# Kernel optimization log

Hardware: AMD Instinct MI355X
Metric: run time of the kernel (lower is better)

Reference implementation:

```python
import jax, jax.numpy as jnp
import numpy as np

B, T, C = 16, 4096, 256


def setup_inputs() -> dict:
    key = jax.random.key(0)
    kx, kl = jax.random.split(key)
    x = jax.random.normal(kx, (B, T, C), dtype=jnp.float32)
    lengths = jax.random.randint(kl, (B,), T // 2, T + 1)  # valid lengths per sample
    pool_ranges = lengths  # region to pool over; k <= pool_range guaranteed by layer/total_layers choice
    return {
        "x": x,
        "lengths": lengths,
        "pool_ranges": pool_ranges,
        "top_k": 4,
        "layer": 1,
        "total_layers": 4,
    }


def _pool_one(xb, k, pool_range):
    # xb: [T, C]; keep, per column independently, the k largest values among the
    # first pool_range rows, preserving original row order (torch kmax_pooling).
    Trows, Ccols = xb.shape
    valid = jnp.arange(Trows) < pool_range            # [T]
    vals = jnp.where(valid[:, None], xb, -jnp.inf)    # mask invalid rows to rank last
    order = jnp.argsort(-vals, axis=0)                # descending order per column
    rank = jnp.argsort(order, axis=0)                 # inverse permutation = rank of each row
    keep = (rank < k) & valid[:, None]                # [T, C] which entries survive
    pos = jnp.cumsum(keep.astype(jnp.int32), axis=0) - 1  # compacted output row per column
    idx = jnp.where(keep, pos, Trows)                 # dropped entries -> dummy row Trows
    cols = jnp.arange(Ccols)[None, :]
    out = jnp.zeros((Trows + 1, Ccols), xb.dtype).at[idx, cols].set(
        jnp.where(keep, xb, jnp.zeros((), xb.dtype))
    )
    return out[:-1]                                   # [T, C]; rows >= k are zero padding


def reference(x, lengths, pool_ranges, top_k, layer, total_layers):
    # pool_target = max(top_k, ceil((total_layers - layer)/total_layers * length))
    num = total_layers - layer
    k = jnp.maximum(top_k, (num * lengths + total_layers - 1) // total_layers)
    k = jnp.minimum(k, pool_ranges)  # topk requires k <= available rows
    results = jax.vmap(_pool_one)(x, k, pool_ranges)  # [B, T, C], zero-padded past k_i
    pool_result_ranges = k
    return results, pool_result_ranges
```

## Files before the change

kernel.cpp:

```cpp
#include <hip/hip_runtime.h>
#include <stdint.h>


constexpr int T_ROWS = 4096;
constexpr int C_COLS = 256;
constexpr int NBATCH = 16;
constexpr int NSUB   = 8;
constexpr size_t NTOT = (size_t)NBATCH * T_ROWS * C_COLS;

__device__ __forceinline__ int compute_k(const int* lengths, const int* pool_ranges,
                                         const int* p_top_k, const int* p_layer,
                                         const int* p_total, int b, int* pr_out)
{
    int pr = pool_ranges[b];
    pr = pr < 0 ? 0 : (pr > T_ROWS ? T_ROWS : pr);
    const int len   = lengths[b];
    const int top_k = p_top_k[0];
    const int tot   = p_total[0];
    const int num   = tot - p_layer[0];
    int k = (num * len + tot - 1) / tot;
    if (k < top_k) k = top_k;
    if (k > pr)    k = pr;
    *pr_out = pr;
    return k;
}

__global__ __launch_bounds__(256)
void transpose_key_kernel(const float* __restrict__ x, uint32_t* __restrict__ xT)
{
    __shared__ uint32_t tile[64][65];
    const int bid = blockIdx.x;
    const int b   = bid >> 8;
    const int tt  = (bid >> 2) & 63;
    const int ct  = bid & 3;
    const int t0  = tt * 64, c0 = ct * 64;
    const int tid = threadIdx.x;
    const int qq  = tid & 15;
    const int rr  = tid >> 4;

    #pragma unroll
    for (int it = 0; it < 4; ++it) {
        const int r = it * 16 + rr;
        const float4 v = *reinterpret_cast<const float4*>(
            x + ((size_t)(b * T_ROWS + t0 + r) << 8) + c0 + qq * 4);
        const uint32_t w4[4] = {__float_as_uint(v.x), __float_as_uint(v.y),
                                __float_as_uint(v.z), __float_as_uint(v.w)};
        #pragma unroll
        for (int j = 0; j < 4; ++j)
            tile[qq * 4 + j][r] = w4[j] ^ ((w4[j] >> 31) ? 0xFFFFFFFFu : 0x80000000u);
    }
    __syncthreads();
    #pragma unroll
    for (int it = 0; it < 4; ++it) {
        const int cl = it * 16 + rr;
        uint4 o;
        o.x = tile[cl][qq * 4 + 0];
        o.y = tile[cl][qq * 4 + 1];
        o.z = tile[cl][qq * 4 + 2];
        o.w = tile[cl][qq * 4 + 3];
        *reinterpret_cast<uint4*>(
            xT + ((size_t)(b * C_COLS + c0 + cl) << 12) + t0 + qq * 4) = o;
    }
}

__global__ __launch_bounds__(256, 5)
void kmax_select_kernel(const uint32_t* __restrict__ xT,
                        const int* __restrict__ lengths,
                        const int* __restrict__ pool_ranges,
                        const int* __restrict__ p_top_k,
                        const int* __restrict__ p_layer,
                        const int* __restrict__ p_total,
                        float* __restrict__ out,
                        float* __restrict__ ws)
{
    __shared__ uint32_t hist[4][256 * NSUB];

    const int t    = threadIdx.x;
    const int lane = t & 63;
    const int wid  = t >> 6;
    const int bid  = blockIdx.x;
    const int b    = bid >> 6;
    const int cg   = bid & 63;
    const int c    = cg * 4 + wid;

    int pr;
    const int k = compute_k(lengths, pool_ranges, p_top_k, p_layer, p_total, b, &pr);

    const uint4* cp = reinterpret_cast<const uint4*>(
                          xT + ((size_t)(b * C_COLS + c) << 12)) + lane;
    uint4 ld[16];
    #pragma unroll
    for (int i = 0; i < 16; ++i) ld[i] = cp[i * 64];

    const int rb = lane * 4;
    uint32_t u[64];
    #pragma unroll
    for (int i = 0; i < 16; ++i) {
        const int rowb = i * 256 + rb;
        u[i * 4 + 0] = (rowb + 0 < pr) ? ld[i].x : 0u;
        u[i * 4 + 1] = (rowb + 1 < pr) ? ld[i].y : 0u;
        u[i * 4 + 2] = (rowb + 2 < pr) ? ld[i].z : 0u;
        u[i * 4 + 3] = (rowb + 3 < pr) ? ld[i].w : 0u;
        asm("" : "+v"(u[i*4+0]), "+v"(u[i*4+1]), "+v"(u[i*4+2]), "+v"(u[i*4+3]));
    }

    if (k > 0) {
        uint32_t* hp = &hist[wid][0];
        uint32_t prefix = 0u, pmask = 0u, rem = (uint32_t)k;
        const uint32_t sub = lane & (NSUB - 1);

        #pragma unroll 1
        for (int pass = 0; pass < 4; ++pass) {
            const int shift = 24 - 8 * pass;
            uint4* hp4 = reinterpret_cast<uint4*>(hp);
            const uint4 z4 = make_uint4(0u, 0u, 0u, 0u);
            #pragma unroll
            for (int z = 0; z < 8; ++z) hp4[z * 64 + lane] = z4;
            #pragma unroll
            for (int m = 0; m < 64; ++m) {
                const uint32_t ui = u[m];
                if ((ui & pmask) == prefix)
                    atomicAdd(&hp[((ui >> shift) & 255u) * NSUB + sub], 1u);
            }
            const uint4* rp = reinterpret_cast<const uint4*>(
                                  &hp[(252 - 4 * lane) * NSUB]);
            uint32_t cnt[4];
            #pragma unroll
            for (int bb = 0; bb < 4; ++bb) {
                const uint4 a = rp[bb * 2 + 0];
                const uint4 d = rp[bb * 2 + 1];
                cnt[bb] = a.x + a.y + a.z + a.w + d.x + d.y + d.z + d.w;
            }
            uint32_t c4[4], loc[4], s = 0;
            #pragma unroll
            for (int q = 0; q < 4; ++q) { c4[q] = cnt[3 - q]; loc[q] = s; s += c4[q]; }
            uint32_t incl = s;
            #pragma unroll
            for (int off = 1; off < 64; off <<= 1) {
                const uint32_t nb = __shfl_up(incl, (unsigned)off, 64);
                if (lane >= off) incl += nb;
            }
            const uint32_t gexcl = incl - s;
            uint32_t sel = 0, nrem = 0;
            bool found = false;
            #pragma unroll
            for (int q = 0; q < 4; ++q) {
                const uint32_t sbb = gexcl + loc[q];
                if (sbb < rem && sbb + c4[q] >= rem) {
                    sel   = 255u - (uint32_t)(4 * lane + q);
                    nrem  = rem - sbb;
                    found = true;
                }
            }
            const unsigned long long fm = __ballot(found);
            const int src = __ffsll(fm) - 1;
            sel  = __shfl(sel,  src, 64);
            nrem = __shfl(nrem, src, 64);
            prefix |= sel << shift;
            pmask  |= 0xFFu << shift;
            rem = nrem;
        }

        const uint32_t th = prefix, tn = rem;
        uint32_t G = 0, E = 0;
        float* dst = ws + ((size_t)(b * C_COLS + c) << 12);
        #pragma unroll
        for (int i = 0; i < 16; ++i) {
            const int rowb = i * 256 + rb;
            uint32_t gt[4], eq[4], pk = 0;
            #pragma unroll
            for (int j = 0; j < 4; ++j) {
                const uint32_t ui = u[i * 4 + j];
                gt[j] = (ui > th) ? 1u : 0u;
                eq[j] = ((rowb + j < pr) && ui == th) ? 1u : 0u;
                pk += (gt[j] << 16) | eq[j];
            }
            uint32_t incl = pk;
            #pragma unroll
            for (int off = 1; off < 64; off <<= 1) {
                const uint32_t nb = __shfl_up(incl, (unsigned)off, 64);
                if (lane >= off) incl += nb;
            }
            const uint32_t tot  = __shfl(incl, 63, 64);
            const uint32_t base = incl - pk;
            uint32_t g = G + (base >> 16), e = E + (base & 0xFFFFu);
            #pragma unroll
            for (int j = 0; j < 4; ++j) {
                if (gt[j] || (eq[j] && e < tn)) {
                    const uint32_t pos  = g + (e < tn ? e : tn);
                    const uint32_t ui   = u[i * 4 + j];
                    const uint32_t bits = ui ^ ((ui >> 31) ? 0x80000000u : 0xFFFFFFFFu);
                    dst[pos] = __uint_as_float(bits);
                }
                g += gt[j];
                e += eq[j];
            }
            G += tot >> 16;
            E += tot & 0xFFFFu;
        }
    }

    if (cg == 0 && t == 0)
        out[NTOT + (size_t)b] = (float)k;
}

__global__ __launch_bounds__(256)
void finalize_kernel(const float* __restrict__ ws,
                     const int* __restrict__ lengths,
                     const int* __restrict__ pool_ranges,
                     const int* __restrict__ p_top_k,
                     const int* __restrict__ p_layer,
                     const int* __restrict__ p_total,
                     float* __restrict__ out)
{
    __shared__ float tile[64][65];
    const int bid  = blockIdx.x;
    const int b    = bid >> 8;
    const int pt   = (bid >> 2) & 63;
    const int ct   = bid & 3;
    const int pos0 = pt * 64, c0 = ct * 64;

    int pr;
    const int k = compute_k(lengths, pool_ranges, p_top_k, p_layer, p_total, b, &pr);

    const int tid = threadIdx.x;
    const int qq  = tid & 15;
    const int rr  = tid >> 4;
    float4* out4 = reinterpret_cast<float4*>(out);
    const float4 z4 = make_float4(0.f, 0.f, 0.f, 0.f);

    if (pos0 < k) {
        const float4* ws4 = reinterpret_cast<const float4*>(ws);
        #pragma unroll
        for (int it = 0; it < 4; ++it) {
            const int cl = it * 16 + rr;
            const float4 v = ws4[((size_t)(b * C_COLS + c0 + cl) << 10)
                                 + (pos0 >> 2) + qq];
            tile[cl][qq * 4 + 0] = v.x;
            tile[cl][qq * 4 + 1] = v.y;
            tile[cl][qq * 4 + 2] = v.z;
            tile[cl][qq * 4 + 3] = v.w;
        }
        __syncthreads();
        #pragma unroll
        for (int it = 0; it < 4; ++it) {
            const int r = it * 16 + rr;
            float4 v;
            v.x = tile[qq * 4 + 0][r];
            v.y = tile[qq * 4 + 1][r];
            v.z = tile[qq * 4 + 2][r];
            v.w = tile[qq * 4 + 3][r];
            if (pos0 + r >= k) v = z4;
            out4[((size_t)(b * T_ROWS + pos0 + r) << 6) + (c0 >> 2) + qq] = v;
        }
    } else {
        #pragma unroll
        for (int it = 0; it < 4; ++it) {
            const int r = it * 16 + rr;
            out4[((size_t)(b * T_ROWS + pos0 + r) << 6) + (c0 >> 2) + qq] = z4;
        }
    }
}

extern "C" void kernel_launch(void* const* d_in, const int* in_sizes, int n_in,
                              void* d_out, int out_size, void* d_ws, size_t ws_size,
                              hipStream_t stream)
{
    const float* x            = (const float*)d_in[0];
    const int*   lengths      = (const int*)d_in[1];
    const int*   pool_ranges  = (const int*)d_in[2];
    const int*   top_k        = (const int*)d_in[3];
    const int*   layer        = (const int*)d_in[4];
    const int*   total_layers = (const int*)d_in[5];
    float*       out          = (float*)d_out;
    float*       ws           = (float*)d_ws;

    hipLaunchKernelGGL(transpose_key_kernel, dim3(4096), dim3(256), 0, stream,
                       x, (uint32_t*)ws);
    hipLaunchKernelGGL(kmax_select_kernel, dim3(1024), dim3(256), 0, stream,
                       (const uint32_t*)ws, lengths, pool_ranges,
                       top_k, layer, total_layers, out, ws);
    hipLaunchKernelGGL(finalize_kernel, dim3(4096), dim3(256), 0, stream,
                       ws, lengths, pool_ranges, top_k, layer, total_layers, out);
}
```

Baseline: 101.0 us.

## Transpose histogram to sub-major layout and software-pipeline column loads

Reorganizes the per-wave radix histogram from bin-major with interleaved sub-copies to sub-copy-major with reversed bin order. This changes the LDS bank pattern of the atomics and lets each lane sum its four bins with contiguous uint4 reads. The 16 upfront vector loads become a rolling four-deep prefetch to cut register pressure, and the occupancy hint drops from 5 to 4 blocks per CU. The sub-copy index now sits in the high address bits, so atomics from lanes in the same sub-group may conflict on banks differently than before.

```diff
diff --git a/kernel.cpp b/kernel.cpp
--- a/kernel.cpp
+++ b/kernel.cpp
@@ -63,7 +63,7 @@
     }
 }
 
-__global__ __launch_bounds__(256, 5)
+__global__ __launch_bounds__(256, 4)
 void kmax_select_kernel(const uint32_t* __restrict__ xT,
                         const int* __restrict__ lengths,
                         const int* __restrict__ pool_ranges,
@@ -73,7 +73,7 @@
                         float* __restrict__ out,
                         float* __restrict__ ws)
 {
-    __shared__ uint32_t hist[4][256 * NSUB];
+    __shared__ uint32_t hist[4][NSUB][256];
 
     const int t    = threadIdx.x;
     const int lane = t & 63;
@@ -88,24 +88,25 @@
 
     const uint4* cp = reinterpret_cast<const uint4*>(
                           xT + ((size_t)(b * C_COLS + c) << 12)) + lane;
-    uint4 ld[16];
-    #pragma unroll
-    for (int i = 0; i < 16; ++i) ld[i] = cp[i * 64];
-
     const int rb = lane * 4;
     uint32_t u[64];
+    uint4 pf[4];
+    #pragma unroll
+    for (int i = 0; i < 4; ++i) pf[i] = cp[i * 64];
     #pragma unroll
     for (int i = 0; i < 16; ++i) {
+        const uint4 v = pf[i & 3];
+        if (i + 4 < 16) pf[i & 3] = cp[(i + 4) * 64];
         const int rowb = i * 256 + rb;
-        u[i * 4 + 0] = (rowb + 0 < pr) ? ld[i].x : 0u;
-        u[i * 4 + 1] = (rowb + 1 < pr) ? ld[i].y : 0u;
-        u[i * 4 + 2] = (rowb + 2 < pr) ? ld[i].z : 0u;
-        u[i * 4 + 3] = (rowb + 3 < pr) ? ld[i].w : 0u;
+        u[i * 4 + 0] = (rowb + 0 < pr) ? v.x : 0u;
+        u[i * 4 + 1] = (rowb + 1 < pr) ? v.y : 0u;
+        u[i * 4 + 2] = (rowb + 2 < pr) ? v.z : 0u;
+        u[i * 4 + 3] = (rowb + 3 < pr) ? v.w : 0u;
         asm("" : "+v"(u[i*4+0]), "+v"(u[i*4+1]), "+v"(u[i*4+2]), "+v"(u[i*4+3]));
     }
 
     if (k > 0) {
-        uint32_t* hp = &hist[wid][0];
+        uint32_t* hp = &hist[wid][0][0];
         uint32_t prefix = 0u, pmask = 0u, rem = (uint32_t)k;
         const uint32_t sub = lane & (NSUB - 1);
 
@@ -120,27 +121,24 @@
             for (int m = 0; m < 64; ++m) {
                 const uint32_t ui = u[m];
                 if ((ui & pmask) == prefix)
-                    atomicAdd(&hp[((ui >> shift) & 255u) * NSUB + sub], 1u);
-            }
-            const uint4* rp = reinterpret_cast<const uint4*>(
-                                  &hp[(252 - 4 * lane) * NSUB]);
-            uint32_t cnt[4];
-            #pragma unroll
-            for (int bb = 0; bb < 4; ++bb) {
-                const uint4 a = rp[bb * 2 + 0];
-                const uint4 d = rp[bb * 2 + 1];
-                cnt[bb] = a.x + a.y + a.z + a.w + d.x + d.y + d.z + d.w;
-            }
-            uint32_t c4[4], loc[4], s = 0;
-            #pragma unroll
-            for (int q = 0; q < 4; ++q) { c4[q] = cnt[3 - q]; loc[q] = s; s += c4[q]; }
-            uint32_t incl = s;
+                    atomicAdd(&hp[sub * 256 + (255u - ((ui >> shift) & 255u))], 1u);
+            }
+            uint32_t c4[4] = {0u, 0u, 0u, 0u};
+            #pragma unroll
+            for (int s = 0; s < NSUB; ++s) {
+                const uint4 a = *reinterpret_cast<const uint4*>(&hp[s * 256 + 4 * lane]);
+                c4[0] += a.x; c4[1] += a.y; c4[2] += a.z; c4[3] += a.w;
+            }
+            uint32_t loc[4], ssum = 0;
+            #pragma unroll
+            for (int q = 0; q < 4; ++q) { loc[q] = ssum; ssum += c4[q]; }
+            uint32_t incl = ssum;
             #pragma unroll
             for (int off = 1; off < 64; off <<= 1) {
                 const uint32_t nb = __shfl_up(incl, (unsigned)off, 64);
                 if (lane >= off) incl += nb;
             }
-            const uint32_t gexcl = incl - s;
+            const uint32_t gexcl = incl - ssum;
             uint32_t sel = 0, nrem = 0;
             bool found = false;
             #pragma unroll
```

Result: faster. 90.70 us (-10.2%).
